# Optimization experiments

Measured on AMD Instinct MI355X. Metric: run time of the kernel, lower is better.

Reference implementation:

```python
import jax, jax.numpy as jnp
import numpy as np

B, N, OBS, H, A = 1024, 64, 128, 256, 16
NH = 4
HD = H // NH


def _linear_params(key, fan_in, fan_out):
    k1, k2 = jax.random.split(key)
    bound = 1.0 / np.sqrt(fan_in)
    W = jax.random.uniform(k1, (fan_out, fan_in), jnp.float32, -bound, bound)
    b = jax.random.uniform(k2, (fan_out,), jnp.float32, -bound, bound)
    return W, b


def setup_inputs() -> dict:
    key = jax.random.key(0)
    ks = jax.random.split(key, 10)
    obs = jax.random.normal(ks[0], (B, N, OBS), jnp.float32)
    adj = jax.random.randint(ks[1], (B, N, N), 0, 2).astype(jnp.float32)
    # guarantee every row has at least one neighbor (self-loop) so softmax is finite
    adj = jnp.maximum(adj, jnp.eye(N, dtype=jnp.float32)[None])
    W1, b1 = _linear_params(ks[2], OBS, H)
    W2, b2 = _linear_params(ks[3], H, H)
    Wq, bq = _linear_params(ks[4], H, H)
    Wk, bk = _linear_params(ks[5], H, H)
    Wv, bv = _linear_params(ks[6], H, H)
    Wo, bo = _linear_params(ks[7], H, H)
    Wc, bc = _linear_params(ks[8], H, H)
    W3, b3 = _linear_params(ks[9], H, A)
    return dict(obs=obs, adj=adj, W1=W1, b1=b1, W2=W2, b2=b2,
                Wq=Wq, bq=bq, Wk=Wk, bk=bk, Wv=Wv, bv=bv,
                Wo=Wo, bo=bo, Wc=Wc, bc=bc, W3=W3, b3=b3)


def reference(obs, adj, W1, b1, W2, b2, Wq, bq, Wk, bk, Wv, bv, Wo, bo, Wc, bc, W3, b3):
    lin = lambda x, W, b: jnp.einsum('bnd,od->bno', x, W) + b
    x = jax.nn.relu(lin(obs, W1, b1))
    x = jax.nn.relu(lin(x, W2, b2))
    # multi-head attention with adjacency mask
    def heads(t):  # [B,N,H] -> [B,NH,N,HD]
        return t.reshape(B, N, NH, HD).transpose(0, 2, 1, 3)
    q = heads(lin(x, Wq, bq))
    k = heads(lin(x, Wk, bk))
    v = heads(lin(x, Wv, bv))
    scores = jnp.einsum('bhqd,bhkd->bhqk', q, k) / np.sqrt(HD).astype(np.float32)
    scores = jnp.where(adj[:, None] == 0, -jnp.inf, scores)
    attn = jax.nn.softmax(scores, axis=-1)
    out = jnp.einsum('bhqk,bhkd->bhqd', attn, v)
    out = out.transpose(0, 2, 1, 3).reshape(B, N, H)
    x = lin(out, Wo, bo)
    # communication: adj @ fc(x)
    x = jnp.einsum('bnm,bmh->bnh', adj, lin(x, Wc, bc))
    return lin(x, W3, b3)
```

## Files before the change

### kernel.cpp

```cpp
#include <hip/hip_runtime.h>
#include <stdint.h>

typedef unsigned short u16;
typedef unsigned long long u64;
typedef __attribute__((ext_vector_type(8))) short short8;
typedef __attribute__((ext_vector_type(4))) float f32x4;

#define MFMA16 __builtin_amdgcn_mfma_f32_16x16x32_bf16

#define MTOT 65536

__device__ __forceinline__ u16 f2bf(float f) {
  union { float f; uint32_t u; } v; v.f = f;
  uint32_t r = v.u + 0x7FFFu + ((v.u >> 16) & 1u);
  return (u16)(r >> 16);
}

union U8 { short8 v; u16 u[8]; };
union U4 { u64 v; u16 u[4]; };

__device__ __forceinline__ void cp16(const void* g, void* l) {
  __builtin_amdgcn_global_load_lds(
      (const __attribute__((address_space(1))) void*)g,
      (__attribute__((address_space(3))) void*)l, 16, 0, 0);
}

__global__ __launch_bounds__(256) void k_l1(
    const float* __restrict__ Wc, const float* __restrict__ Wo,
    const float* __restrict__ bo, const float* __restrict__ bc,
    float* __restrict__ M1, float* __restrict__ bv,
    const float* __restrict__ W1, const float* __restrict__ W2,
    const float* __restrict__ Wq, const float* __restrict__ Wk,
    u16* o1, u16* o2, u16* oq, u16* ok) {
  const int bid = blockIdx.x, tid = threadIdx.x;
  if (bid < 256) {
    __shared__ float wcr[256];
    __shared__ float red[4];
    const int j = bid, d = tid;
    wcr[d] = Wc[j * 256 + d];
    __syncthreads();
    float acc = 0.f;
    for (int i = 0; i < 256; i++) acc += wcr[i] * Wo[i * 256 + d];
    M1[j * 256 + d] = acc;
    float p = wcr[d] * bo[d];
    for (int off = 32; off >= 1; off >>= 1) p += __shfl_xor(p, off);
    if ((d & 63) == 0) red[d >> 6] = p;
    __syncthreads();
    if (d == 0) bv[j] = bc[j] + red[0] + red[1] + red[2] + red[3];
  } else {
    int off8 = (bid - 256) * 256 + tid;
    const float* src; u16* dst;
    if      (off8 <  4096) { src = W1; dst = o1; }
    else if (off8 < 12288) { src = W2; dst = o2; off8 -= 4096; }
    else if (off8 < 20480) { src = Wq; dst = oq; off8 -= 12288; }
    else                   { src = Wk; dst = ok; off8 -= 20480; }
    const int e = off8 * 8;
    f32x4 a = *(const f32x4*)(src + e);
    f32x4 b = *(const f32x4*)(src + e + 4);
    U8 pk;
#pragma unroll
    for (int j = 0; j < 4; j++) { pk.u[j] = f2bf(a[j]); pk.u[4 + j] = f2bf(b[j]); }
    *(short8*)(dst + e) = pk.v;
  }
}

template<int K, bool AF32>
__device__ __forceinline__ void gemm_full2(
    const void* __restrict__ Ain, const u16* __restrict__ W,
    const float* __restrict__ bias, u16* __restrict__ C,
    const int m0, const bool relu, char* smem) {
  const int tid = threadIdx.x;
  const int lane = tid & 63, wid = tid >> 6;
  const int wr = wid >> 1, wc = wid & 1;
  const int ro = lane & 15, hi = lane >> 4;

  f32x4 acc0[4][4], acc1[4][4];
#pragma unroll
  for (int m = 0; m < 4; m++)
#pragma unroll
    for (int n = 0; n < 4; n++) {
      acc0[m][n] = (f32x4){0.f, 0.f, 0.f, 0.f};
      acc1[m][n] = (f32x4){0.f, 0.f, 0.f, 0.f};
    }

  auto stage = [&](int buf, int k0) {
    char* Ax = smem + buf * 24576;
    char* Bx = Ax + 8192;
    if (AF32) {
      const float* Af = (const float*)Ain;
#pragma unroll
      for (int it = 0; it < 2; it++) {
        const int e = (tid + it * 256) * 8;
        const int r = e >> 5, c = e & 31;
        const float* s = Af + (size_t)(m0 + r) * K + k0 + c;
        f32x4 a = *(const f32x4*)s, b = *(const f32x4*)(s + 4);
        U8 pk;
#pragma unroll
        for (int j = 0; j < 4; j++) { pk.u[j] = f2bf(a[j]); pk.u[4 + j] = f2bf(b[j]); }
        *(short8*)(Ax + ((r * 64 + c * 2) ^ ((r & 3) << 4))) = pk.v;
      }
    } else {
      const u16* Ab = (const u16*)Ain;
#pragma unroll
      for (int i = 0; i < 2; i++) {
        const int boff = i * 4096 + wid * 1024;
        const int t = boff + lane * 16;
        const int row = t >> 6;
        const int cb = (t & 63) ^ ((row & 3) << 4);
        cp16(Ab + (size_t)(m0 + row) * K + k0 + (cb >> 1), Ax + boff);
      }
    }
#pragma unroll
    for (int i = 0; i < 4; i++) {
      const int boff = i * 4096 + wid * 1024;
      const int t = boff + lane * 16;
      const int row = t >> 6;
      const int cb = (t & 63) ^ ((row & 3) << 4);
      cp16(W + (size_t)row * K + k0 + (cb >> 1), Bx + boff);
    }
  };

  auto compute = [&](int buf) {
    char* Ax = smem + buf * 24576;
    char* Bx = Ax + 8192;
    short8 af[4], fb0[4], fb1[4];
#pragma unroll
    for (int m = 0; m < 4; m++) {
      const int row = wr * 64 + m * 16 + ro;
      af[m] = *(const short8*)(Ax + ((row * 64 + hi * 16) ^ ((row & 3) << 4)));
    }
#pragma unroll
    for (int n = 0; n < 4; n++) {
      const int r0 = wc * 64 + n * 16 + ro;
      fb0[n] = *(const short8*)(Bx + ((r0 * 64 + hi * 16) ^ ((r0 & 3) << 4)));
      const int r1 = 128 + r0;
      fb1[n] = *(const short8*)(Bx + ((r1 * 64 + hi * 16) ^ ((r1 & 3) << 4)));
    }
    __builtin_amdgcn_s_setprio(1);
#pragma unroll
    for (int m = 0; m < 4; m++)
#pragma unroll
      for (int n = 0; n < 4; n++) {
        acc0[m][n] = MFMA16(af[m], fb0[n], acc0[m][n], 0, 0, 0);
        acc1[m][n] = MFMA16(af[m], fb1[n], acc1[m][n], 0, 0, 0);
      }
    __builtin_amdgcn_s_setprio(0);
  };

  stage(0, 0);
  __syncthreads();
  int cur = 0;
  for (int k0 = 32; k0 < K; k0 += 32) {
    stage(cur ^ 1, k0);
    compute(cur);
    __syncthreads();
    cur ^= 1;
  }
  compute(cur);
  __syncthreads();

  u16 (*Cs)[136] = (u16(*)[136])smem;
  auto ep = [&](f32x4 (&acc)[4][4], const int n0) {
#pragma unroll
    for (int half = 0; half < 2; half++) {
      if (wr == half) {
#pragma unroll
        for (int n = 0; n < 4; n++) {
          const int col = wc * 64 + n * 16 + ro;
          const float bb = bias[n0 + col];
#pragma unroll
          for (int m = 0; m < 4; m++)
#pragma unroll
            for (int j = 0; j < 4; j++) {
              float val = acc[m][n][j] + bb;
              if (relu) val = fmaxf(val, 0.f);
              Cs[m * 16 + hi * 4 + j][col] = f2bf(val);
            }
        }
      }
      __syncthreads();
      for (int i = tid; i < 64 * 16; i += 256) {
        const int r = i >> 4, c = (i & 15) << 3;
        *(short8*)(C + (size_t)(m0 + half * 64 + r) * 256 + n0 + c) = *(short8*)&Cs[r][c];
      }
      __syncthreads();
    }
  };
  ep(acc0, 0);
  ep(acc1, 128);
}

__global__ __launch_bounds__(256, 2) void k_gemm1_prep2(
    const float* __restrict__ obs, const u16* __restrict__ W1b,
    const float* __restrict__ b1, u16* __restrict__ x1,
    const float* __restrict__ W3, const float* __restrict__ M1,
    const float* __restrict__ bvchain, const float* __restrict__ bvw,
    float* __restrict__ Wzf, float* __restrict__ bz) {
  __shared__ char smem[49152];
  if (blockIdx.x < 512) {
    gemm_full2<128, true>(obs, W1b, b1, x1, (int)blockIdx.x * 128, true, smem);
    return;
  }
  float* w3r = (float*)smem;
  float* red = (float*)(smem + 1024);
  const int a = blockIdx.x - 512, d = threadIdx.x;
  w3r[d] = W3[a * 256 + d];
  __syncthreads();
  float acc = 0.f;
  for (int j = 0; j < 256; j++) acc += w3r[j] * M1[j * 256 + d];
  Wzf[a * 256 + d] = acc;
  float p = w3r[d] * bvchain[d] + acc * bvw[d];
  for (int off = 32; off >= 1; off >>= 1) p += __shfl_xor(p, off);
  if ((d & 63) == 0) red[d >> 6] = p;
  __syncthreads();
  if (d == 0) bz[a] = red[0] + red[1] + red[2] + red[3];
}

__global__ __launch_bounds__(256, 2) void k_x2_prep3(
    const u16* __restrict__ x1, const u16* __restrict__ W2b,
    const float* __restrict__ b2, u16* __restrict__ x2,
    const float* __restrict__ Wzf, const float* __restrict__ Wv,
    u16* __restrict__ G) {
  __shared__ char smem[49152];
  if (blockIdx.x < 512) {
    gemm_full2<256, false>(x1, W2b, b2, x2, (int)blockIdx.x * 128, true, smem);
    return;
  }
  const int g = blockIdx.x - 512, d2 = threadIdx.x;
  const int h = g >> 4, a = g & 15;
  float* wzr = (float*)smem;
  if (d2 < 64) wzr[d2] = Wzf[a * 256 + h * 64 + d2];
  __syncthreads();
  float acc = 0.f;
#pragma unroll 8
  for (int d = 0; d < 64; d++) acc += wzr[d] * Wv[(size_t)(h * 64 + d) * 256 + d2];
  G[g * 256 + d2] = f2bf(acc);
}

__global__ __launch_bounds__(256, 2) void k_qk_gemmv(
    const u16* __restrict__ x2,
    const u16* __restrict__ Wqb, const float* __restrict__ bq, u16* __restrict__ Qg,
    const u16* __restrict__ Wkb, const float* __restrict__ bk, u16* __restrict__ Kg,
    const u16* __restrict__ G, u16* __restrict__ Vzt) {
  __shared__ char smem[49152];
  const int bid = blockIdx.x;
  if (bid < 1024) {
    const int q = bid >> 4, r = bid & 15;
    const int mt = q * 8 + (r & 7);
    const int sub = r >> 3;
    gemm_full2<256, false>(x2, sub ? Wkb : Wqb, sub ? bk : bq, sub ? Kg : Qg,
                           mt * 128, false, smem);
    return;
  }
  const int tid = threadIdx.x;
  const int lane = tid & 63, w = tid >> 6;
  const int ro = lane & 15, hi = lane >> 4;
  const int m0 = (bid - 1024) * 128;

  f32x4 acc[2][4];
#pragma unroll
  for (int m = 0; m < 2; m++)
#pragma unroll
    for (int n = 0; n < 4; n++) acc[m][n] = (f32x4){0.f, 0.f, 0.f, 0.f};

  auto stage = [&](int buf, int k0) {
    char* Ax = smem + buf * 12288;
    char* Bx = Ax + 8192;
#pragma unroll
    for (int i = 0; i < 2; i++) {
      const int boff = i * 4096 + w * 1024;
      const int t = boff + lane * 16;
      const int row = t >> 6;
      const int cb = (t & 63) ^ ((row & 3) << 4);
      cp16(x2 + (size_t)(m0 + row) * 256 + k0 + (cb >> 1), Ax + boff);
    }
    {
      const int boff = w * 1024;
      const int t = boff + lane * 16;
      const int row = t >> 6;
      const int cb = (t & 63) ^ ((row & 3) << 4);
      cp16(G + (size_t)row * 256 + k0 + (cb >> 1), Bx + boff);
    }
  };
  auto compute = [&](int buf) {
    char* Ax = smem + buf * 12288;
    char* Bx = Ax + 8192;
    short8 af[2], fb[4];
#pragma unroll
    for (int m = 0; m < 2; m++) {
      const int row = w * 32 + m * 16 + ro;
      af[m] = *(const short8*)(Ax + ((row * 64 + hi * 16) ^ ((row & 3) << 4)));
    }
#pragma unroll
    for (int n = 0; n < 4; n++) {
      const int row = n * 16 + ro;
      fb[n] = *(const short8*)(Bx + ((row * 64 + hi * 16) ^ ((row & 3) << 4)));
    }
    __builtin_amdgcn_s_setprio(1);
#pragma unroll
    for (int m = 0; m < 2; m++)
#pragma unroll
      for (int n = 0; n < 4; n++)
        acc[m][n] = MFMA16(af[m], fb[n], acc[m][n], 0, 0, 0);
    __builtin_amdgcn_s_setprio(0);
  };

  stage(0, 0);
  __syncthreads();
  int cur = 0;
  for (int k0 = 32; k0 < 256; k0 += 32) {
    stage(cur ^ 1, k0);
    compute(cur);
    __syncthreads();
    cur ^= 1;
  }
  compute(cur);

#pragma unroll
  for (int m = 0; m < 2; m++) {
    const int rbase = w * 32 + m * 16;
    const int bidx = (m0 >> 6) + (rbase >> 6);
    const int ke = (rbase + hi * 4) & 63;
#pragma unroll
    for (int n = 0; n < 4; n++) {
      const int c = n * 16 + ro;
      U4 pk;
#pragma unroll
      for (int j = 0; j < 4; j++) pk.u[j] = f2bf(acc[m][n][j]);
      *(u64*)(Vzt + (size_t)bidx * 4096 + (size_t)c * 64 + ke) = pk.v;
    }
  }
}

__global__ __launch_bounds__(256, 2) void attn_fused(
    const u16* __restrict__ Qg, const u16* __restrict__ Kg,
    const u16* __restrict__ Vzt, const float* __restrict__ adj,
    const float* __restrict__ bz, const float* __restrict__ b3,
    float* __restrict__ out) {
  __shared__ u16 Ps[4][64][72];
  __shared__ float Zs[4][64][16];
  __shared__ u64 adjm[64];
  __shared__ u16 chunk[64][4];

  const int b = blockIdx.x, tid = threadIdx.x;
  const int lane = tid & 63, w = tid >> 6;
  const int ro = lane & 15, hi = lane >> 4;
  const int hc = w * 64;
  const size_t base = (size_t)b * 64 * 256;

  short8 kb[4][2];
#pragma unroll
  for (int n = 0; n < 4; n++)
#pragma unroll
    for (int ks = 0; ks < 2; ks++)
      kb[n][ks] = *(const short8*)(Kg + base + (size_t)(n * 16 + ro) * 256 + hc + ks * 32 + hi * 8);

  {
    const int q = tid >> 2, qa = tid & 3;
    const float* ar = adj + ((size_t)b * 64 + q) * 64 + qa * 16;
    f32x4 a0 = *(const f32x4*)(ar);
    f32x4 a1 = *(const f32x4*)(ar + 4);
    f32x4 a2 = *(const f32x4*)(ar + 8);
    f32x4 a3 = *(const f32x4*)(ar + 12);
    unsigned m16 = 0;
#pragma unroll
    for (int i = 0; i < 4; i++) {
      m16 |= (unsigned)(a0[i] != 0.f) << i;
      m16 |= (unsigned)(a1[i] != 0.f) << (4 + i);
      m16 |= (unsigned)(a2[i] != 0.f) << (8 + i);
      m16 |= (unsigned)(a3[i] != 0.f) << (12 + i);
    }
    chunk[q][qa] = (u16)m16;
  }

  f32x4 s[4][4];
#pragma unroll
  for (int m = 0; m < 4; m++) {
    short8 af[2];
#pragma unroll
    for (int ks = 0; ks < 2; ks++)
      af[ks] = *(const short8*)(Qg + base + (size_t)(m * 16 + ro) * 256 + hc + ks * 32 + hi * 8);
#pragma unroll
    for (int n = 0; n < 4; n++) s[m][n] = (f32x4){0.f, 0.f, 0.f, 0.f};
#pragma unroll
    for (int ks = 0; ks < 2; ks++)
#pragma unroll
      for (int n = 0; n < 4; n++)
        s[m][n] = MFMA16(af[ks], kb[n][ks], s[m][n], 0, 0, 0);
  }

  short8 vz[2];
#pragma unroll
  for (int ks = 0; ks < 2; ks++)
    vz[ks] = *(const short8*)(Vzt + (size_t)b * 4096 + (size_t)(hc / 4 + ro) * 64 + ks * 32 + hi * 8);

  __syncthreads();
  if (tid < 64)
    adjm[tid] = (u64)chunk[tid][0] | ((u64)chunk[tid][1] << 16) |
                ((u64)chunk[tid][2] << 32) | ((u64)chunk[tid][3] << 48);
  __syncthreads();

#pragma unroll
  for (int m = 0; m < 4; m++) {
#pragma unroll
    for (int j = 0; j < 4; j++) {
      const int q = m * 16 + hi * 4 + j;
      const u64 msk = adjm[q];
      float sv[4], ev[4];
      float mx = -3.0e38f;
#pragma unroll
      for (int n = 0; n < 4; n++) {
        const bool on = (msk >> (n * 16 + ro)) & 1ull;
        sv[n] = on ? s[m][n][j] * 0.125f : -3.0e38f;
        mx = fmaxf(mx, sv[n]);
      }
      mx = fmaxf(mx, __shfl_xor(mx, 1));
      mx = fmaxf(mx, __shfl_xor(mx, 2));
      mx = fmaxf(mx, __shfl_xor(mx, 4));
      mx = fmaxf(mx, __shfl_xor(mx, 8));
      float sum = 0.f;
#pragma unroll
      for (int n = 0; n < 4; n++) {
        ev[n] = (sv[n] > -1.0e37f) ? __expf(sv[n] - mx) : 0.f;
        sum += ev[n];
      }
      sum += __shfl_xor(sum, 1);
      sum += __shfl_xor(sum, 2);
      sum += __shfl_xor(sum, 4);
      sum += __shfl_xor(sum, 8);
      const float inv = 1.0f / sum;
#pragma unroll
      for (int n = 0; n < 4; n++)
        Ps[w][q][n * 16 + ro] = f2bf(ev[n] * inv);
    }
  }

#pragma unroll
  for (int m = 0; m < 4; m++) {
    short8 pa[2];
    pa[0] = *(const short8*)&Ps[w][m * 16 + ro][hi * 8];
    pa[1] = *(const short8*)&Ps[w][m * 16 + ro][32 + hi * 8];
    f32x4 oz = (f32x4){0.f, 0.f, 0.f, 0.f};
#pragma unroll
    for (int ks = 0; ks < 2; ks++)
      oz = MFMA16(pa[ks], vz[ks], oz, 0, 0, 0);
#pragma unroll
    for (int j = 0; j < 4; j++)
      Zs[w][m * 16 + hi * 4 + j][ro] = oz[j];
  }
  __syncthreads();

  for (int i = tid; i < 1024; i += 256) {
    const int r = i >> 4, a = i & 15;
    Zs[0][r][a] += Zs[1][r][a] + Zs[2][r][a] + Zs[3][r][a];
  }
  __syncthreads();

  {
    const int n = tid >> 2, a4 = (tid & 3) << 2;
    const u64 msk = adjm[n];
    const float deg = (float)__popcll(msk);
    float a0 = 0.f, a1 = 0.f, a2 = 0.f, a3 = 0.f;
#pragma unroll 8
    for (int m = 0; m < 64; m++) {
      const float wv = (float)((msk >> m) & 1ull);
      f32x4 z = *(const f32x4*)&Zs[0][m][a4];
      a0 += wv * z[0]; a1 += wv * z[1]; a2 += wv * z[2]; a3 += wv * z[3];
    }
    f32x4 r;
    r[0] = a0 + b3[a4 + 0] + deg * bz[a4 + 0];
    r[1] = a1 + b3[a4 + 1] + deg * bz[a4 + 1];
    r[2] = a2 + b3[a4 + 2] + deg * bz[a4 + 2];
    r[3] = a3 + b3[a4 + 3] + deg * bz[a4 + 3];
    *(f32x4*)(out + ((size_t)b * 64 + n) * 16 + a4) = r;
  }
}

extern "C" void kernel_launch(void* const* d_in, const int* in_sizes, int n_in,
                              void* d_out, int out_size, void* d_ws, size_t ws_size,
                              hipStream_t stream) {
  const float* obs = (const float*)d_in[0];
  const float* adj = (const float*)d_in[1];
  const float* W1  = (const float*)d_in[2];
  const float* b1  = (const float*)d_in[3];
  const float* W2  = (const float*)d_in[4];
  const float* b2  = (const float*)d_in[5];
  const float* Wq  = (const float*)d_in[6];
  const float* bq  = (const float*)d_in[7];
  const float* Wk  = (const float*)d_in[8];
  const float* bk  = (const float*)d_in[9];
  const float* Wv  = (const float*)d_in[10];
  const float* bvw = (const float*)d_in[11];
  const float* Wo  = (const float*)d_in[12];
  const float* bo  = (const float*)d_in[13];
  const float* Wc  = (const float*)d_in[14];
  const float* bc  = (const float*)d_in[15];
  const float* W3  = (const float*)d_in[16];
  const float* b3  = (const float*)d_in[17];
  float* out = (float*)d_out;

  char* ws = (char*)d_ws;
  const size_t BIG = (size_t)MTOT * 256 * 2;
  u16* buf0 = (u16*)(ws);
  u16* buf1 = (u16*)(ws + BIG);
  u16* buf2 = (u16*)(ws + 2 * BIG);
  u16* buf3 = (u16*)(ws + 3 * BIG);
  char* p = ws + 4 * BIG;
  u16* W1b = (u16*)p;              p += 128 * 256 * 2;
  u16* W2b = (u16*)p;              p += 256 * 256 * 2;
  u16* Wqb = (u16*)p;              p += 256 * 256 * 2;
  u16* Wkb = (u16*)p;              p += 256 * 256 * 2;
  float* M1 = (float*)p;           p += 256 * 256 * 4;
  float* Wzf = (float*)p;          p += 16 * 256 * 4;
  u16* G   = (u16*)p;              p += 64 * 256 * 2;
  float* bv = (float*)p;           p += 256 * 4;
  float* bz = (float*)p;           p += 16 * 4;

  dim3 blk(256);
  k_l1<<<dim3(368), blk, 0, stream>>>(Wc, Wo, bo, bc, M1, bv,
                                      W1, W2, Wq, Wk, W1b, W2b, Wqb, Wkb);
  k_gemm1_prep2<<<dim3(528), blk, 0, stream>>>(obs, W1b, b1, buf0,
                                               W3, M1, bv, bvw, Wzf, bz);
  k_x2_prep3<<<dim3(576), blk, 0, stream>>>(buf0, W2b, b2, buf1, Wzf, Wv, G);
  k_qk_gemmv<<<dim3(1536), blk, 0, stream>>>(buf1, Wqb, bq, buf2,
                                             Wkb, bk, buf3, G, buf0);
  attn_fused<<<dim3(1024), blk, 0, stream>>>(buf2, buf3, buf0, adj, bz, b3, out);
}
```

Measured before the change: 122.5 us.

## Prefetch two stages ahead with vmcnt waits and change LDS swizzle

```diff
diff --git a/kernel.cpp b/kernel.cpp
--- a/kernel.cpp
+++ b/kernel.cpp
@@ -24,6 +24,8 @@
       (const __attribute__((address_space(1))) void*)g,
       (__attribute__((address_space(3))) void*)l, 16, 0, 0);
 }
+
+__device__ __forceinline__ int swz(int row) { return ((row >> 1) & 3) << 4; }
 
 __global__ __launch_bounds__(256) void k_l1(
     const float* __restrict__ Wc, const float* __restrict__ Wo,
@@ -97,7 +99,7 @@
         U8 pk;
 #pragma unroll
         for (int j = 0; j < 4; j++) { pk.u[j] = f2bf(a[j]); pk.u[4 + j] = f2bf(b[j]); }
-        *(short8*)(Ax + ((r * 64 + c * 2) ^ ((r & 3) << 4))) = pk.v;
+        *(short8*)(Ax + ((r * 64 + c * 2) ^ swz(r))) = pk.v;
       }
     } else {
       const u16* Ab = (const u16*)Ain;
@@ -106,7 +108,7 @@
         const int boff = i * 4096 + wid * 1024;
         const int t = boff + lane * 16;
         const int row = t >> 6;
-        const int cb = (t & 63) ^ ((row & 3) << 4);
+        const int cb = (t & 63) ^ swz(row);
         cp16(Ab + (size_t)(m0 + row) * K + k0 + (cb >> 1), Ax + boff);
       }
     }
@@ -115,7 +117,7 @@
       const int boff = i * 4096 + wid * 1024;
       const int t = boff + lane * 16;
       const int row = t >> 6;
-      const int cb = (t & 63) ^ ((row & 3) << 4);
+      const int cb = (t & 63) ^ swz(row);
       cp16(W + (size_t)row * K + k0 + (cb >> 1), Bx + boff);
     }
   };
@@ -127,14 +129,14 @@
 #pragma unroll
     for (int m = 0; m < 4; m++) {
       const int row = wr * 64 + m * 16 + ro;
-      af[m] = *(const short8*)(Ax + ((row * 64 + hi * 16) ^ ((row & 3) << 4)));
+      af[m] = *(const short8*)(Ax + ((row * 64 + hi * 16) ^ swz(row)));
     }
 #pragma unroll
     for (int n = 0; n < 4; n++) {
       const int r0 = wc * 64 + n * 16 + ro;
-      fb0[n] = *(const short8*)(Bx + ((r0 * 64 + hi * 16) ^ ((r0 & 3) << 4)));
+      fb0[n] = *(const short8*)(Bx + ((r0 * 64 + hi * 16) ^ swz(r0)));
       const int r1 = 128 + r0;
-      fb1[n] = *(const short8*)(Bx + ((r1 * 64 + hi * 16) ^ ((r1 & 3) << 4)));
+      fb1[n] = *(const short8*)(Bx + ((r1 * 64 + hi * 16) ^ swz(r1)));
     }
     __builtin_amdgcn_s_setprio(1);
 #pragma unroll
@@ -147,17 +149,32 @@
     __builtin_amdgcn_s_setprio(0);
   };
 
-  stage(0, 0);
-  __syncthreads();
-  int cur = 0;
-  for (int k0 = 32; k0 < K; k0 += 32) {
-    stage(cur ^ 1, k0);
+  constexpr int NT = K / 32;
+  if (AF32) {
+    stage(0, 0);
+    __syncthreads();
+    int cur = 0;
+    for (int k0 = 32; k0 < K; k0 += 32) {
+      stage(cur ^ 1, k0);
+      compute(cur);
+      __syncthreads();
+      cur ^= 1;
+    }
     compute(cur);
     __syncthreads();
-    cur ^= 1;
-  }
-  compute(cur);
-  __syncthreads();
+  } else {
+    stage(0, 0);
+    stage(1, 32);
+#pragma unroll
+    for (int t = 0; t < NT; ++t) {
+      if (t == NT - 1) asm volatile("s_waitcnt vmcnt(0)" ::: "memory");
+      else             asm volatile("s_waitcnt vmcnt(6)" ::: "memory");
+      asm volatile("s_barrier" ::: "memory");
+      compute(t & 1);
+      asm volatile("s_barrier" ::: "memory");
+      if (t + 2 < NT) stage(t & 1, (t + 2) * 32);
+    }
+  }
 
   u16 (*Cs)[136] = (u16(*)[136])smem;
   auto ep = [&](f32x4 (&acc)[4][4], const int n0) {
@@ -271,14 +288,14 @@
       const int boff = i * 4096 + w * 1024;
       const int t = boff + lane * 16;
       const int row = t >> 6;
-      const int cb = (t & 63) ^ ((row & 3) << 4);
+      const int cb = (t & 63) ^ swz(row);
       cp16(x2 + (size_t)(m0 + row) * 256 + k0 + (cb >> 1), Ax + boff);
     }
     {
       const int boff = w * 1024;
       const int t = boff + lane * 16;
       const int row = t >> 6;
-      const int cb = (t & 63) ^ ((row & 3) << 4);
+      const int cb = (t & 63) ^ swz(row);
       cp16(G + (size_t)row * 256 + k0 + (cb >> 1), Bx + boff);
     }
   };
@@ -289,12 +306,12 @@
 #pragma unroll
     for (int m = 0; m < 2; m++) {
       const int row = w * 32 + m * 16 + ro;
-      af[m] = *(const short8*)(Ax + ((row * 64 + hi * 16) ^ ((row & 3) << 4)));
+      af[m] = *(const short8*)(Ax + ((row * 64 + hi * 16) ^ swz(row)));
     }
 #pragma unroll
     for (int n = 0; n < 4; n++) {
       const int row = n * 16 + ro;
-      fb[n] = *(const short8*)(Bx + ((row * 64 + hi * 16) ^ ((row & 3) << 4)));
+      fb[n] = *(const short8*)(Bx + ((row * 64 + hi * 16) ^ swz(row)));
     }
     __builtin_amdgcn_s_setprio(1);
 #pragma unroll
@@ -306,15 +323,16 @@
   };
 
   stage(0, 0);
-  __syncthreads();
-  int cur = 0;
-  for (int k0 = 32; k0 < 256; k0 += 32) {
-    stage(cur ^ 1, k0);
-    compute(cur);
-    __syncthreads();
-    cur ^= 1;
-  }
-  compute(cur);
+  stage(1, 32);
+#pragma unroll
+  for (int t = 0; t < 8; ++t) {
+    if (t == 7) asm volatile("s_waitcnt vmcnt(0)" ::: "memory");
+    else        asm volatile("s_waitcnt vmcnt(3)" ::: "memory");
+    asm volatile("s_barrier" ::: "memory");
+    compute(t & 1);
+    asm volatile("s_barrier" ::: "memory");
+    if (t + 2 < 8) stage(t & 1, (t + 2) * 32);
+  }
 
 #pragma unroll
   for (int m = 0; m < 2; m++) {
```

After: 120.6 us. No clear change (-1.5%).
